# Kernel optimization log

Hardware: AMD Instinct MI355X
Metric: run time of the kernel (lower is better)

The kernel has to match this reference:

```python
import jax, jax.numpy as jnp
import numpy as np
import math

H, E, HD = 12, 768, 64   # heads, embed_dim, per-head hidden
B, S, L = 8, 512, 512    # batch, dec len, enc len
EPS = 1e-12


def layer_norm(x, w, b):
    u = jnp.mean(x, axis=-1, keepdims=True)
    s = jnp.mean((x - u) ** 2, axis=-1, keepdims=True)
    return w * (x - u) / jnp.sqrt(s + EPS) + b


def gelu(x):
    return x * 0.5 * (1.0 + jax.lax.erf(x / math.sqrt(2.0)))


def attention(k, q, w_k, w_q, pw, pb, mask):
    # k:[b,kl,E] q:[b,ql,E] w_k/w_q:[H,E,HD] mask broadcastable to [b,H,ql,kl]
    kx = jnp.einsum('ble,hed->bhld', k, w_k)
    qx = jnp.einsum('bqe,hed->bhqd', q, w_q)
    score = jnp.einsum('bhqd,bhkd->bhqk', qx, kx) / math.sqrt(HD)
    score = jnp.where(mask, score, jnp.asarray(-1e4, score.dtype))
    attn = jax.nn.softmax(score, axis=-1)
    out = jnp.einsum('bhqk,bhkd->bhqd', attn, kx)  # values are kx (as in source)
    b_, h, ql, d = out.shape
    out = out.transpose(0, 2, 1, 3).reshape(b_, ql, h * d)
    return out @ pw + pb


def setup_inputs() -> dict:
    key = jax.random.key(0)
    ks = jax.random.split(key, 16)
    xav = lambda k, shp, fan: jax.random.normal(k, shp, jnp.float32) * math.sqrt(2.0 / fan)
    inp = {
        'X': jax.random.normal(ks[0], (B, S, E), jnp.float32),
        'enc_outputs': jax.random.normal(ks[1], (B, L, E), jnp.float32),
        'enc_valid_lens': jax.random.randint(ks[2], (B,), 1, L + 1, jnp.int32),
        'w_kx1': xav(ks[3], (H, E, HD), E + HD),
        'w_qx1': xav(ks[4], (H, E, HD), E + HD),
        'proj1_w': xav(ks[5], (H * HD, E), 2 * E),
        'proj1_b': jnp.zeros((E,), jnp.float32),
        'ln1_w': jnp.ones((E,), jnp.float32),
        'ln1_b': jnp.zeros((E,), jnp.float32),
        'w_kx2': xav(ks[6], (H, E, HD), E + HD),
        'w_qx2': xav(ks[7], (H, E, HD), E + HD),
        'proj2_w': xav(ks[8], (H * HD, E), 2 * E),
        'proj2_b': jnp.zeros((E,), jnp.float32),
        'ln2_w': jnp.ones((E,), jnp.float32),
        'ln2_b': jnp.zeros((E,), jnp.float32),
        'ffn_w1': xav(ks[9], (E, E), 2 * E),
        'ffn_b1': jnp.zeros((E,), jnp.float32),
        'ffn_w2': xav(ks[10], (E, E), 2 * E),
        'ffn_b2': jnp.zeros((E,), jnp.float32),
        'ln3_w': jnp.ones((E,), jnp.float32),
        'ln3_b': jnp.zeros((E,), jnp.float32),
    }
    return inp


def reference(X, enc_outputs, enc_valid_lens,
              w_kx1, w_qx1, proj1_w, proj1_b, ln1_w, ln1_b,
              w_kx2, w_qx2, proj2_w, proj2_b, ln2_w, ln2_b,
              ffn_w1, ffn_b1, ffn_w2, ffn_b2, ln3_w, ln3_b):
    s = X.shape[1]
    # training path: dec_valid_lens is 2D -> causal mask in Attention
    causal = jnp.tril(jnp.ones((s, s), dtype=bool))[None, None]          # [1,1,s,s]
    X2 = attention(X, X, w_kx1, w_qx1, proj1_w, proj1_b, causal)
    Y = layer_norm(X2 + X, ln1_w, ln1_b)
    # cross mask: key padding from enc_valid_lens (1D branch)
    kl = enc_outputs.shape[1]
    pad = (jnp.arange(kl)[None] < enc_valid_lens[:, None])[:, None, None]  # [b,1,1,kl]
    Y2 = attention(enc_outputs, Y, w_kx2, w_qx2, proj2_w, proj2_b, pad)
    Z = layer_norm(Y2 + Y, ln2_w, ln2_b)
    F = gelu(Z @ ffn_w1 + ffn_b1) @ ffn_w2 + ffn_b2
    return layer_norm(F + Z, ln3_w, ln3_b)
```

## Files before the change

### kernel.cpp

```cpp
#include <hip/hip_runtime.h>
#include <hip/hip_bf16.h>

typedef __hip_bfloat16 bf16;
typedef __attribute__((ext_vector_type(8))) short s8v;
typedef __attribute__((ext_vector_type(4))) short s4v;
typedef __attribute__((ext_vector_type(4))) float f4v;

#define H_ 12
#define E_ 768
#define HD_ 64
#define B_ 8
#define S_ 512
#define M_ 4096

struct P9 { const void* s[8]; bf16* d[8]; const void* vs[10]; bf16* vd[10]; };

typedef __attribute__((address_space(3))) void lds_void;
typedef const __attribute__((address_space(1))) void g_void;

__device__ __forceinline__ void async_copy16(const bf16* g, short* l) {
    __builtin_amdgcn_global_load_lds((g_void*)g, (lds_void*)l, 16, 0, 0);
}

__device__ __forceinline__ float sh2f(short v) {
    unsigned int u = ((unsigned int)(unsigned short)v) << 16;
    return __uint_as_float(u);
}

__device__ __forceinline__ short f2sh(float v) {
    bf16 b = __float2bfloat16(v);
    return *(short*)&b;
}

__global__ void detect_kernel(const unsigned int* __restrict__ X, int* flag) {
    __shared__ int cnt;
    if (threadIdx.x == 0) cnt = 0;
    __syncthreads();
    int good = 0;
    for (int i = threadIdx.x; i < 16384; i += 256) {
        unsigned e = (X[i] >> 7) & 0xFFu;
        good += (e >= 100u && e <= 141u) ? 1 : 0;
    }
    atomicAdd(&cnt, good);
    __syncthreads();
    if (threadIdx.x == 0) *flag = (cnt > 9830) ? 0 : 1;
}

__global__ void conv2_kernel(const void* s0, const void* s1, bf16* d0, bf16* d1,
                             const int* __restrict__ flag) {
    const int fp32 = *flag;
    const void* s = blockIdx.y ? s1 : s0;
    bf16* d = blockIdx.y ? d1 : d0;
    int i = (blockIdx.x * 256 + threadIdx.x) * 4;
    if (fp32) {
        float4 v = *(const float4*)((const float*)s + i);
        bf16 a = __float2bfloat16(v.x), b = __float2bfloat16(v.y),
             c = __float2bfloat16(v.z), e = __float2bfloat16(v.w);
        s4v o = { *(short*)&a, *(short*)&b, *(short*)&c, *(short*)&e };
        *(s4v*)(d + i) = o;
    } else {
        *(s4v*)(d + i) = *(const s4v*)((const bf16*)s + i);
    }
}

__device__ __forceinline__ bf16 ldcvt(const void* s, int i, int fp32) {
    return fp32 ? __float2bfloat16(((const float*)s)[i]) : ((const bf16*)s)[i];
}

__global__ void repack_kernel(P9 p, const int* __restrict__ flag) {
    const int fp32 = *flag;
    const int z = blockIdx.z;
    if (z == 8) {
        int id = blockIdx.y * 12 + blockIdx.x;
        if (id < 10) {
            const void* s = p.vs[id];
            bf16* d = p.vd[id];
            for (int i = threadIdx.x; i < E_; i += 256) d[i] = ldcvt(s, i, fp32);
        }
        return;
    }
    __shared__ float t[64][65];
    const int c = threadIdx.x & 63, r0 = threadIdx.x >> 6;
    if (z < 4) {
        const void* s = p.s[z];
        bf16* d = p.d[z];
        const int e0 = blockIdx.x * 64, h = blockIdx.y;
        #pragma unroll
        for (int j = 0; j < 16; ++j) {
            int r = r0 * 16 + j;
            int idx = (h * E_ + e0 + r) * HD_ + c;
            t[r][c] = fp32 ? ((const float*)s)[idx] : __bfloat162float(((const bf16*)s)[idx]);
        }
        __syncthreads();
        #pragma unroll
        for (int j = 0; j < 16; ++j) {
            int r = r0 * 16 + j;
            d[(size_t)(h * 64 + r) * E_ + e0 + c] = __float2bfloat16(t[c][r]);
        }
    } else {
        const void* s = p.s[z];
        bf16* d = p.d[z];
        const int k0 = blockIdx.x * 64, n0 = blockIdx.y * 64;
        #pragma unroll
        for (int j = 0; j < 16; ++j) {
            int r = r0 * 16 + j;
            int idx = (k0 + r) * E_ + n0 + c;
            t[r][c] = fp32 ? ((const float*)s)[idx] : __bfloat162float(((const bf16*)s)[idx]);
        }
        __syncthreads();
        #pragma unroll
        for (int j = 0; j < 16; ++j) {
            int r = r0 * 16 + j;
            d[(size_t)(n0 + r) * E_ + k0 + c] = __float2bfloat16(t[c][r]);
        }
    }
}

template <int EPI>
__global__ __launch_bounds__(256, 4) void gemm3(const bf16* __restrict__ A,
                                                const bf16* __restrict__ Bt,
                                                bf16* __restrict__ C,
                                                const bf16* __restrict__ bias,
                                                const bf16* __restrict__ res) {
    __shared__ short As[64 * 64];
    __shared__ short Bs[64 * 64];
    const int bm = blockIdx.x, bn = blockIdx.y;
    const int tid = threadIdx.x;
    const int w = tid >> 6, l = tid & 63;
    const int wr = (w >> 1) * 32, wc = (w & 1) * 32;
    const int lc = l & 15, quad = l >> 4;
    const int srA = l >> 3, slot = l & 7;
    const int kc = (slot ^ srA) * 8;

    f4v acc[2][2] = {};

    for (int k0 = 0; k0 < E_; k0 += 64) {
        #pragma unroll
        for (int c = 0; c < 2; ++c) {
            int seg = w * 2 + c;
            int row = seg * 8 + srA;
            async_copy16(A + (size_t)(bm * 64 + row) * E_ + k0 + kc, &As[seg * 512]);
            async_copy16(Bt + (size_t)(bn * 64 + row) * E_ + k0 + kc, &Bs[seg * 512]);
        }
        __syncthreads();

        #pragma unroll
        for (int kk = 0; kk < 2; ++kk) {
            s8v a[2], b[2];
            #pragma unroll
            for (int t = 0; t < 2; ++t) {
                int ar = wr + t * 16 + lc;
                a[t] = *(const s8v*)&As[ar * 64 + (((kk * 4 + quad) ^ (ar & 7)) * 8)];
                int bc = wc + t * 16 + lc;
                b[t] = *(const s8v*)&Bs[bc * 64 + (((kk * 4 + quad) ^ (bc & 7)) * 8)];
            }
            acc[0][0] = __builtin_amdgcn_mfma_f32_16x16x32_bf16(a[0], b[0], acc[0][0], 0, 0, 0);
            acc[0][1] = __builtin_amdgcn_mfma_f32_16x16x32_bf16(a[0], b[1], acc[0][1], 0, 0, 0);
            acc[1][0] = __builtin_amdgcn_mfma_f32_16x16x32_bf16(a[1], b[0], acc[1][0], 0, 0, 0);
            acc[1][1] = __builtin_amdgcn_mfma_f32_16x16x32_bf16(a[1], b[1], acc[1][1], 0, 0, 0);
        }
        __syncthreads();
    }

    #pragma unroll
    for (int mt = 0; mt < 2; ++mt)
        #pragma unroll
        for (int nt = 0; nt < 2; ++nt)
            #pragma unroll
            for (int i = 0; i < 4; ++i) {
                int row = bm * 64 + wr + mt * 16 + quad * 4 + i;
                int col = bn * 64 + wc + nt * 16 + lc;
                float v = acc[mt][nt][i];
                if (EPI == 1)
                    v += __bfloat162float(bias[col]) + __bfloat162float(res[(size_t)row * E_ + col]);
                if (EPI == 2) {
                    v += __bfloat162float(bias[col]);
                    v = 0.5f * v * (1.0f + erff(v * 0.70710678118654752f));
                }
                C[(size_t)row * E_ + col] = __float2bfloat16(v);
            }
}

__global__ __launch_bounds__(256, 4) void gemm3q(const bf16* __restrict__ Xc,
                                                 const bf16* __restrict__ ENCc,
                                                 const bf16* __restrict__ Bt,
                                                 bf16* __restrict__ K1,
                                                 bf16* __restrict__ Q1,
                                                 bf16* __restrict__ K2,
                                                 bf16* __restrict__ KT1,
                                                 bf16* __restrict__ KT2) {
    __shared__ short sm[8192];
    short* As = sm;
    short* Bs = sm + 4096;
    const int bm = blockIdx.x, bn = blockIdx.y;
    const int tid = threadIdx.x;
    const int w = tid >> 6, l = tid & 63;
    const int wr = (w >> 1) * 32, wc = (w & 1) * 32;
    const int lc = l & 15, quad = l >> 4;
    const int srA = l >> 3, slot = l & 7;
    const int kc = (slot ^ srA) * 8;

    const bf16* A = (bn >= 24) ? ENCc : Xc;

    f4v acc[2][2] = {};

    for (int k0 = 0; k0 < E_; k0 += 64) {
        #pragma unroll
        for (int c = 0; c < 2; ++c) {
            int seg = w * 2 + c;
            int row = seg * 8 + srA;
            async_copy16(A + (size_t)(bm * 64 + row) * E_ + k0 + kc, &As[seg * 512]);
            async_copy16(Bt + (size_t)(bn * 64 + row) * E_ + k0 + kc, &Bs[seg * 512]);
        }
        __syncthreads();

        #pragma unroll
        for (int kk = 0; kk < 2; ++kk) {
            s8v a[2], b[2];
            #pragma unroll
            for (int t = 0; t < 2; ++t) {
                int ar = wr + t * 16 + lc;
                a[t] = *(const s8v*)&As[ar * 64 + (((kk * 4 + quad) ^ (ar & 7)) * 8)];
                int bc = wc + t * 16 + lc;
                b[t] = *(const s8v*)&Bs[bc * 64 + (((kk * 4 + quad) ^ (bc & 7)) * 8)];
            }
            acc[0][0] = __builtin_amdgcn_mfma_f32_16x16x32_bf16(a[0], b[0], acc[0][0], 0, 0, 0);
            acc[0][1] = __builtin_amdgcn_mfma_f32_16x16x32_bf16(a[0], b[1], acc[0][1], 0, 0, 0);
            acc[1][0] = __builtin_amdgcn_mfma_f32_16x16x32_bf16(a[1], b[0], acc[1][0], 0, 0, 0);
            acc[1][1] = __builtin_amdgcn_mfma_f32_16x16x32_bf16(a[1], b[1], acc[1][1], 0, 0, 0);
        }
        __syncthreads();
    }

    const int band = (bn < 12) ? 0 : (bn < 24) ? 1 : 2;
    const int nb = bn - band * 12;
    bf16* C = (band == 0) ? K1 : (band == 1) ? Q1 : K2;

    #pragma unroll
    for (int mt = 0; mt < 2; ++mt)
        #pragma unroll
        for (int nt = 0; nt < 2; ++nt)
            #pragma unroll
            for (int i = 0; i < 4; ++i) {
                int row = bm * 64 + wr + mt * 16 + quad * 4 + i;
                int col = nb * 64 + wc + nt * 16 + lc;
                C[(size_t)row * E_ + col] = __float2bfloat16(acc[mt][nt][i]);
            }

    if (band != 1) {
        bf16* KT = (band == 0) ? KT1 : KT2;
        #pragma unroll
        for (int mt = 0; mt < 2; ++mt)
            #pragma unroll
            for (int nt = 0; nt < 2; ++nt)
                #pragma unroll
                for (int i = 0; i < 4; ++i) {
                    int srow = wr + mt * 16 + quad * 4 + i;
                    int d = wc + nt * 16 + lc;
                    sm[d * 72 + srow] = f2sh(acc[mt][nt][i]);
                }
        __syncthreads();
        const int drow = tid >> 2, c0 = (tid & 3) * 16;
        s8v o0 = *(const s8v*)&sm[drow * 72 + c0];
        s8v o1 = *(const s8v*)&sm[drow * 72 + c0 + 8];
        const int b = bm >> 3, s0 = (bm & 7) * 64;
        bf16* dp = KT + ((size_t)((b * H_ + nb) * 64 + drow) * S_) + s0 + c0;
        *(s8v*)dp = o0;
        *(s8v*)(dp + 8) = o1;
    }
}

template <bool CAUSAL>
__global__ __launch_bounds__(256) void attn_kernel(const bf16* __restrict__ Q,
                                                   const bf16* __restrict__ Kx,
                                                   const bf16* __restrict__ KT,
                                                   bf16* __restrict__ O,
                                                   const int* __restrict__ vlen) {
    __shared__ short qs[64 * 64];
    __shared__ short ks[64 * 64];
    __shared__ short kts[64 * 64];
    __shared__ short ps[64 * 72];

    const int bh = blockIdx.x, qt = blockIdx.y;
    const int h = bh % H_, b = bh / H_;
    const int tid = threadIdx.x, w = tid >> 6, l = tid & 63;
    const int lr = (l >> 4) * 4, lc = l & 15, quad = l >> 4;
    const int srA = l >> 3, slot = l & 7;
    const int kc = (slot ^ srA) * 8;
    const int rq = w * 16 + lc;

    #pragma unroll
    for (int c = 0; c < 2; ++c) {
        int seg = w * 2 + c;
        int row = seg * 8 + srA;
        async_copy16(Q + ((size_t)(b * S_ + qt * 64 + row) * H_ + h) * HD_ + kc, &qs[seg * 512]);
    }

    const int valid = CAUSAL ? S_ : vlen[b];
    const int kmax = CAUSAL ? (qt + 1) : ((valid + 63) >> 6);

    float m_i[4], l_i[4];
    for (int i = 0; i < 4; i++) { m_i[i] = -3.0e38f; l_i[i] = 0.0f; }
    f4v o_acc[4] = {};
    s8v aq0, aq1;

    for (int kt = 0; kt < kmax; ++kt) {
        #pragma unroll
        for (int c = 0; c < 2; ++c) {
            int seg = w * 2 + c;
            int row = seg * 8 + srA;
            async_copy16(Kx + ((size_t)(b * S_ + kt * 64 + row) * H_ + h) * HD_ + kc, &ks[seg * 512]);
            async_copy16(KT + (size_t)(bh * 64 + row) * S_ + kt * 64 + kc, &kts[seg * 512]);
        }
        __syncthreads();

        if (kt == 0) {
            aq0 = *(const s8v*)&qs[rq * 64 + ((quad ^ (rq & 7)) * 8)];
            aq1 = *(const s8v*)&qs[rq * 64 + (((4 + quad) ^ (rq & 7)) * 8)];
        }

        f4v sacc[4] = {};
        #pragma unroll
        for (int nt = 0; nt < 4; nt++) {
            int rk = nt * 16 + lc;
            s8v bk0 = *(const s8v*)&ks[rk * 64 + ((quad ^ (rk & 7)) * 8)];
            s8v bk1 = *(const s8v*)&ks[rk * 64 + (((4 + quad) ^ (rk & 7)) * 8)];
            sacc[nt] = __builtin_amdgcn_mfma_f32_16x16x32_bf16(aq0, bk0, sacc[nt], 0, 0, 0);
            sacc[nt] = __builtin_amdgcn_mfma_f32_16x16x32_bf16(aq1, bk1, sacc[nt], 0, 0, 0);
        }

        #pragma unroll
        for (int i = 0; i < 4; i++) {
            int qabs = qt * 64 + w * 16 + lr + i;
            float sv[4];
            float mx = -3.0e38f;
            #pragma unroll
            for (int nt = 0; nt < 4; nt++) {
                int kabs = kt * 64 + nt * 16 + lc;
                float s = sacc[nt][i] * 0.125f;
                bool ok = CAUSAL ? (kabs <= qabs) : (kabs < valid);
                sv[nt] = ok ? s : -1.0e4f;
                mx = fmaxf(mx, sv[nt]);
            }
            #pragma unroll
            for (int off = 1; off < 16; off <<= 1) mx = fmaxf(mx, __shfl_xor(mx, off));
            float mnew = fmaxf(m_i[i], mx);
            float alpha = __expf(m_i[i] - mnew);
            float psum = 0.0f;
            #pragma unroll
            for (int nt = 0; nt < 4; nt++) {
                float p = __expf(sv[nt] - mnew);
                psum += p;
                ps[(w * 16 + lr + i) * 72 + nt * 16 + lc] = f2sh(p);
            }
            #pragma unroll
            for (int off = 1; off < 16; off <<= 1) psum += __shfl_xor(psum, off);
            l_i[i] = l_i[i] * alpha + psum;
            m_i[i] = mnew;
            #pragma unroll
            for (int dt = 0; dt < 4; dt++) o_acc[dt][i] *= alpha;
        }

        s8v ap0 = *(const s8v*)&ps[rq * 72 + quad * 8];
        s8v ap1 = *(const s8v*)&ps[rq * 72 + 32 + quad * 8];
        #pragma unroll
        for (int dt = 0; dt < 4; dt++) {
            int rd = dt * 16 + lc;
            s8v bv0 = *(const s8v*)&kts[rd * 64 + ((quad ^ (rd & 7)) * 8)];
            s8v bv1 = *(const s8v*)&kts[rd * 64 + (((4 + quad) ^ (rd & 7)) * 8)];
            o_acc[dt] = __builtin_amdgcn_mfma_f32_16x16x32_bf16(ap0, bv0, o_acc[dt], 0, 0, 0);
            o_acc[dt] = __builtin_amdgcn_mfma_f32_16x16x32_bf16(ap1, bv1, o_acc[dt], 0, 0, 0);
        }
        __syncthreads();
    }

    #pragma unroll
    for (int dt = 0; dt < 4; dt++)
        #pragma unroll
        for (int i = 0; i < 4; i++) {
            int q = qt * 64 + w * 16 + lr + i;
            int d = dt * 16 + lc;
            float v = o_acc[dt][i] / l_i[i];
            O[((size_t)(b * S_ + q) * H_ + h) * HD_ + d] = __float2bfloat16(v);
        }
}

__global__ __launch_bounds__(256) void ln2_kernel(const bf16* __restrict__ X,
                                                  const bf16* __restrict__ wv,
                                                  const bf16* __restrict__ bv,
                                                  bf16* __restrict__ outb,
                                                  float* __restrict__ outf,
                                                  const int* __restrict__ flag) {
    const int row = blockIdx.x * 4 + (threadIdx.x >> 6);
    const int l = threadIdx.x & 63;
    const bf16* xr = X + (size_t)row * E_;
    s8v v8 = *(const s8v*)(xr + l * 8);
    s4v v4 = *(const s4v*)(xr + 512 + l * 4);
    float x[12];
    #pragma unroll
    for (int j = 0; j < 8; ++j) x[j] = sh2f(v8[j]);
    #pragma unroll
    for (int j = 0; j < 4; ++j) x[8 + j] = sh2f(v4[j]);
    float s = 0.f, ss = 0.f;
    #pragma unroll
    for (int j = 0; j < 12; ++j) { s += x[j]; ss += x[j] * x[j]; }
    #pragma unroll
    for (int off = 1; off < 64; off <<= 1) {
        s += __shfl_xor(s, off);
        ss += __shfl_xor(ss, off);
    }
    float mu = s * (1.0f / E_);
    float var = ss * (1.0f / E_) - mu * mu;
    float rstd = rsqrtf(fmaxf(var, 0.0f) + 1e-12f);
    const bool f32out = (outf != nullptr) && (*flag != 0);
    #pragma unroll
    for (int j = 0; j < 12; ++j) {
        int c = (j < 8) ? (l * 8 + j) : (512 + l * 4 + (j - 8));
        float v = (x[j] - mu) * rstd * __bfloat162float(wv[c]) + __bfloat162float(bv[c]);
        if (f32out) outf[(size_t)row * E_ + c] = v;
        else        outb[(size_t)row * E_ + c] = __float2bfloat16(v);
    }
}

extern "C" void kernel_launch(void* const* d_in, const int* in_sizes, int n_in,
                              void* d_out, int out_size, void* d_ws, size_t ws_size,
                              hipStream_t stream) {
    const void* X = d_in[0];
    const void* enc = d_in[1];
    const int* vlen = (const int*)d_in[2];

    char* ws = (char*)d_ws;
    int* flag = (int*)ws;
    bf16* vecs = (bf16*)(ws + 256);
    char* wbase = ws + 16384;
    const size_t WSZ = (size_t)E_ * E_ * sizeof(bf16);
    bf16* wk1 = (bf16*)(wbase + 0 * WSZ);
    bf16* wq1 = (bf16*)(wbase + 1 * WSZ);
    bf16* wk2 = (bf16*)(wbase + 2 * WSZ);
    bf16* wq2 = (bf16*)(wbase + 3 * WSZ);
    bf16* p1t = (bf16*)(wbase + 4 * WSZ);
    bf16* p2t = (bf16*)(wbase + 5 * WSZ);
    bf16* f1t = (bf16*)(wbase + 6 * WSZ);
    bf16* f2t = (bf16*)(wbase + 7 * WSZ);
    const size_t ASZ = (size_t)M_ * E_ * sizeof(bf16);
    char* abase = wbase + 8 * WSZ;
    bf16* Xc   = (bf16*)(abase + 0 * ASZ);
    bf16* ENCc = (bf16*)(abase + 1 * ASZ);
    bf16* A0  = (bf16*)(abase + 2 * ASZ);
    bf16* A1  = (bf16*)(abase + 3 * ASZ);
    bf16* A2  = (bf16*)(abase + 4 * ASZ);
    bf16* A3  = (bf16*)(abase + 5 * ASZ);
    bf16* A4  = (bf16*)(abase + 6 * ASZ);
    bf16* A5  = (bf16*)(abase + 7 * ASZ);
    bf16* KT1 = (bf16*)(abase + 8 * ASZ);
    bf16* KT2 = (bf16*)(abase + 9 * ASZ);

    bf16* bias1 = vecs + 0 * E_;
    bf16* lw1   = vecs + 1 * E_;
    bf16* lb1   = vecs + 2 * E_;
    bf16* bias2 = vecs + 3 * E_;
    bf16* lw2   = vecs + 4 * E_;
    bf16* lb2   = vecs + 5 * E_;
    bf16* fb1   = vecs + 6 * E_;
    bf16* fb2   = vecs + 7 * E_;
    bf16* lw3   = vecs + 8 * E_;
    bf16* lb3   = vecs + 9 * E_;

    detect_kernel<<<1, 256, 0, stream>>>((const unsigned int*)X, flag);
    conv2_kernel<<<dim3(M_ * E_ / 1024, 2), 256, 0, stream>>>(X, enc, Xc, ENCc, flag);

    P9 rp;
    rp.s[0] = d_in[3];  rp.d[0] = wk1;
    rp.s[1] = d_in[4];  rp.d[1] = wq1;
    rp.s[2] = d_in[9];  rp.d[2] = wk2;
    rp.s[3] = d_in[10]; rp.d[3] = wq2;
    rp.s[4] = d_in[5];  rp.d[4] = p1t;
    rp.s[5] = d_in[11]; rp.d[5] = p2t;
    rp.s[6] = d_in[15]; rp.d[6] = f1t;
    rp.s[7] = d_in[17]; rp.d[7] = f2t;
    rp.vs[0] = d_in[6];  rp.vd[0] = bias1;
    rp.vs[1] = d_in[7];  rp.vd[1] = lw1;
    rp.vs[2] = d_in[8];  rp.vd[2] = lb1;
    rp.vs[3] = d_in[12]; rp.vd[3] = bias2;
    rp.vs[4] = d_in[13]; rp.vd[4] = lw2;
    rp.vs[5] = d_in[14]; rp.vd[5] = lb2;
    rp.vs[6] = d_in[16]; rp.vd[6] = fb1;
    rp.vs[7] = d_in[18]; rp.vd[7] = fb2;
    rp.vs[8] = d_in[19]; rp.vd[8] = lw3;
    rp.vs[9] = d_in[20]; rp.vd[9] = lb3;
    repack_kernel<<<dim3(12, 12, 9), 256, 0, stream>>>(rp, flag);

    gemm3q<<<dim3(64, 36), 256, 0, stream>>>(Xc, ENCc, wk1, A0, A1, A4, KT1, KT2);

    attn_kernel<true><<<dim3(96, 8), 256, 0, stream>>>(A1, A0, KT1, A2, nullptr);
    gemm3<1><<<dim3(64, 12), 256, 0, stream>>>(A2, p1t, A3, bias1, Xc);
    ln2_kernel<<<M_ / 4, 256, 0, stream>>>(A3, lw1, lb1, A5, nullptr, flag);

    gemm3<0><<<dim3(64, 12), 256, 0, stream>>>(A5, wq2, A1, nullptr, nullptr);
    attn_kernel<false><<<dim3(96, 8), 256, 0, stream>>>(A1, A4, KT2, A2, vlen);
    gemm3<1><<<dim3(64, 12), 256, 0, stream>>>(A2, p2t, A3, bias2, A5);
    ln2_kernel<<<M_ / 4, 256, 0, stream>>>(A3, lw2, lb2, A0, nullptr, flag);

    gemm3<2><<<dim3(64, 12), 256, 0, stream>>>(A0, f1t, A1, fb1, nullptr);
    gemm3<1><<<dim3(64, 12), 256, 0, stream>>>(A1, f2t, A2, fb2, A0);
    ln2_kernel<<<M_ / 4, 256, 0, stream>>>(A2, lw3, lb3, (bf16*)d_out, (float*)d_out, flag);
}
```

Before: 294.1 us.

## Fuse prep kernels and inline cross-attention Q projection into attention kernel

Merges dtype detection, input conversion and weight repacking into one prep kernel. Each block now recomputes the fp32 detection from a reduced 256-word sample instead of reading a flag written by a separate kernel. The cross-attention Q projection GEMM is folded into the attention kernel, which computes its 64x64 Q tile from the LayerNorm output and Wq via MFMA before the KV loop. This removes several launches and one activation round trip through global memory. In exchange, the smaller detection sample changes the heuristic, and each attention block repeats the 768-deep projection without sharing it.

```diff
diff --git a/kernel.cpp b/kernel.cpp
--- a/kernel.cpp
+++ b/kernel.cpp
@@ -32,59 +32,67 @@
     return *(short*)&b;
 }
 
-__global__ void detect_kernel(const unsigned int* __restrict__ X, int* flag) {
-    __shared__ int cnt;
-    if (threadIdx.x == 0) cnt = 0;
+__device__ __forceinline__ int detect_fp32(const unsigned int* __restrict__ Xh,
+                                           int tid, int* scratch) {
+    unsigned e = (Xh[tid] >> 7) & 0xFFu;
+    int good = (e >= 100u && e <= 141u) ? 1 : 0;
+    #pragma unroll
+    for (int off = 1; off < 64; off <<= 1) good += __shfl_xor(good, off);
+    if ((tid & 63) == 0) scratch[tid >> 6] = good;
     __syncthreads();
-    int good = 0;
-    for (int i = threadIdx.x; i < 16384; i += 256) {
-        unsigned e = (X[i] >> 7) & 0xFFu;
-        good += (e >= 100u && e <= 141u) ? 1 : 0;
-    }
-    atomicAdd(&cnt, good);
-    __syncthreads();
-    if (threadIdx.x == 0) *flag = (cnt > 9830) ? 0 : 1;
-}
-
-__global__ void conv2_kernel(const void* s0, const void* s1, bf16* d0, bf16* d1,
-                             const int* __restrict__ flag) {
-    const int fp32 = *flag;
-    const void* s = blockIdx.y ? s1 : s0;
-    bf16* d = blockIdx.y ? d1 : d0;
-    int i = (blockIdx.x * 256 + threadIdx.x) * 4;
-    if (fp32) {
-        float4 v = *(const float4*)((const float*)s + i);
-        bf16 a = __float2bfloat16(v.x), b = __float2bfloat16(v.y),
-             c = __float2bfloat16(v.z), e = __float2bfloat16(v.w);
-        s4v o = { *(short*)&a, *(short*)&b, *(short*)&c, *(short*)&e };
-        *(s4v*)(d + i) = o;
-    } else {
-        *(s4v*)(d + i) = *(const s4v*)((const bf16*)s + i);
-    }
+    int total = scratch[0] + scratch[1] + scratch[2] + scratch[3];
+    return (total <= 154) ? 1 : 0;
 }
 
 __device__ __forceinline__ bf16 ldcvt(const void* s, int i, int fp32) {
     return fp32 ? __float2bfloat16(((const float*)s)[i]) : ((const bf16*)s)[i];
 }
 
-__global__ void repack_kernel(P9 p, const int* __restrict__ flag) {
-    const int fp32 = *flag;
-    const int z = blockIdx.z;
+__global__ __launch_bounds__(256) void prep_kernel(const void* X, const void* enc,
+                                                   bf16* Xc, bf16* ENCc,
+                                                   P9 p) {
+    __shared__ int dsc[4];
+    __shared__ float t[64][65];
+    const int tid = threadIdx.x;
+    const int fp32 = detect_fp32((const unsigned int*)X, tid, dsc);
+    const int id = blockIdx.x;
+
+    if (id < 6144) {
+        const void* s = (id < 3072) ? X : enc;
+        bf16* d = (id < 3072) ? Xc : ENCc;
+        int cid = (id < 3072) ? id : id - 3072;
+        int i = (cid * 256 + tid) * 4;
+        if (fp32) {
+            float4 v = *(const float4*)((const float*)s + i);
+            bf16 a = __float2bfloat16(v.x), b = __float2bfloat16(v.y),
+                 c = __float2bfloat16(v.z), e = __float2bfloat16(v.w);
+            s4v o = { *(short*)&a, *(short*)&b, *(short*)&c, *(short*)&e };
+            *(s4v*)(d + i) = o;
+        } else {
+            *(s4v*)(d + i) = *(const s4v*)((const bf16*)s + i);
+        }
+        return;
+    }
+
+    int id2 = id - 6144;
+    const int z = id2 / 144;
+    const int rem = id2 % 144;
+    const int bx = rem % 12, by = rem / 12;
+
     if (z == 8) {
-        int id = blockIdx.y * 12 + blockIdx.x;
-        if (id < 10) {
-            const void* s = p.vs[id];
-            bf16* d = p.vd[id];
-            for (int i = threadIdx.x; i < E_; i += 256) d[i] = ldcvt(s, i, fp32);
+        int vid = by * 12 + bx;
+        if (vid < 10) {
+            const void* s = p.vs[vid];
+            bf16* d = p.vd[vid];
+            for (int i = tid; i < E_; i += 256) d[i] = ldcvt(s, i, fp32);
         }
         return;
     }
-    __shared__ float t[64][65];
-    const int c = threadIdx.x & 63, r0 = threadIdx.x >> 6;
+    const int c = tid & 63, r0 = tid >> 6;
     if (z < 4) {
         const void* s = p.s[z];
         bf16* d = p.d[z];
-        const int e0 = blockIdx.x * 64, h = blockIdx.y;
+        const int e0 = bx * 64, h = by;
         #pragma unroll
         for (int j = 0; j < 16; ++j) {
             int r = r0 * 16 + j;
@@ -100,7 +108,7 @@
     } else {
         const void* s = p.s[z];
         bf16* d = p.d[z];
-        const int k0 = blockIdx.x * 64, n0 = blockIdx.y * 64;
+        const int k0 = bx * 64, n0 = by * 64;
         #pragma unroll
         for (int j = 0; j < 16; ++j) {
             int r = r0 * 16 + j;
@@ -270,8 +278,9 @@
     }
 }
 
-template <bool CAUSAL>
+template <bool CAUSAL, bool INLQ>
 __global__ __launch_bounds__(256) void attn_kernel(const bf16* __restrict__ Q,
+                                                   const bf16* __restrict__ Wq,
                                                    const bf16* __restrict__ Kx,
                                                    const bf16* __restrict__ KT,
                                                    bf16* __restrict__ O,
@@ -289,11 +298,55 @@
     const int kc = (slot ^ srA) * 8;
     const int rq = w * 16 + lc;
 
-    #pragma unroll
-    for (int c = 0; c < 2; ++c) {
-        int seg = w * 2 + c;
-        int row = seg * 8 + srA;
-        async_copy16(Q + ((size_t)(b * S_ + qt * 64 + row) * H_ + h) * HD_ + kc, &qs[seg * 512]);
+    if (INLQ) {
+        const int wr = (w >> 1) * 32, wc = (w & 1) * 32;
+        const bf16* Arow = Q + (size_t)(b * S_ + qt * 64) * E_;
+        const bf16* Brow = Wq + (size_t)(h * 64) * E_;
+        f4v qacc[2][2] = {};
+        for (int k0 = 0; k0 < E_; k0 += 64) {
+            #pragma unroll
+            for (int c = 0; c < 2; ++c) {
+                int seg = w * 2 + c;
+                int row = seg * 8 + srA;
+                async_copy16(Arow + (size_t)row * E_ + k0 + kc, &ks[seg * 512]);
+                async_copy16(Brow + (size_t)row * E_ + k0 + kc, &kts[seg * 512]);
+            }
+            __syncthreads();
+            #pragma unroll
+            for (int kk = 0; kk < 2; ++kk) {
+                s8v a[2], bb[2];
+                #pragma unroll
+                for (int t = 0; t < 2; ++t) {
+                    int ar = wr + t * 16 + lc;
+                    a[t] = *(const s8v*)&ks[ar * 64 + (((kk * 4 + quad) ^ (ar & 7)) * 8)];
+                    int bc = wc + t * 16 + lc;
+                    bb[t] = *(const s8v*)&kts[bc * 64 + (((kk * 4 + quad) ^ (bc & 7)) * 8)];
+                }
+                qacc[0][0] = __builtin_amdgcn_mfma_f32_16x16x32_bf16(a[0], bb[0], qacc[0][0], 0, 0, 0);
+                qacc[0][1] = __builtin_amdgcn_mfma_f32_16x16x32_bf16(a[0], bb[1], qacc[0][1], 0, 0, 0);
+                qacc[1][0] = __builtin_amdgcn_mfma_f32_16x16x32_bf16(a[1], bb[0], qacc[1][0], 0, 0, 0);
+                qacc[1][1] = __builtin_amdgcn_mfma_f32_16x16x32_bf16(a[1], bb[1], qacc[1][1], 0, 0, 0);
+            }
+            __syncthreads();
+        }
+        #pragma unroll
+        for (int mt = 0; mt < 2; ++mt)
+            #pragma unroll
+            for (int nt = 0; nt < 2; ++nt)
+                #pragma unroll
+                for (int i = 0; i < 4; ++i) {
+                    int row = wr + mt * 16 + quad * 4 + i;
+                    int d = wc + nt * 16 + lc;
+                    qs[row * 64 + (((d >> 3) ^ (row & 7)) * 8) + (d & 7)] = f2sh(qacc[mt][nt][i]);
+                }
+        __syncthreads();
+    } else {
+        #pragma unroll
+        for (int c = 0; c < 2; ++c) {
+            int seg = w * 2 + c;
+            int row = seg * 8 + srA;
+            async_copy16(Q + ((size_t)(b * S_ + qt * 64 + row) * H_ + h) * HD_ + kc, &qs[seg * 512]);
+        }
     }
 
     const int valid = CAUSAL ? S_ : vlen[b];
@@ -390,7 +443,11 @@
                                                   const bf16* __restrict__ bv,
                                                   bf16* __restrict__ outb,
                                                   float* __restrict__ outf,
-                                                  const int* __restrict__ flag) {
+                                                  const unsigned int* __restrict__ Xhead) {
+    __shared__ int dsc[4];
+    int f32out = 0;
+    if (outf != nullptr)
+        f32out = detect_fp32(Xhead, threadIdx.x, dsc);
     const int row = blockIdx.x * 4 + (threadIdx.x >> 6);
     const int l = threadIdx.x & 63;
     const bf16* xr = X + (size_t)row * E_;
@@ -412,7 +469,6 @@
     float mu = s * (1.0f / E_);
     float var = ss * (1.0f / E_) - mu * mu;
     float rstd = rsqrtf(fmaxf(var, 0.0f) + 1e-12f);
-    const bool f32out = (outf != nullptr) && (*flag != 0);
     #pragma unroll
     for (int j = 0; j < 12; ++j) {
         int c = (j < 8) ? (l * 8 + j) : (512 + l * 4 + (j - 8));
@@ -430,7 +486,6 @@
     const int* vlen = (const int*)d_in[2];
 
     char* ws = (char*)d_ws;
-    int* flag = (int*)ws;
     bf16* vecs = (bf16*)(ws + 256);
     char* wbase = ws + 16384;
     const size_t WSZ = (size_t)E_ * E_ * sizeof(bf16);
@@ -466,9 +521,6 @@
     bf16* lw3   = vecs + 8 * E_;
     bf16* lb3   = vecs + 9 * E_;
 
-    detect_kernel<<<1, 256, 0, stream>>>((const unsigned int*)X, flag);
-    conv2_kernel<<<dim3(M_ * E_ / 1024, 2), 256, 0, stream>>>(X, enc, Xc, ENCc, flag);
-
     P9 rp;
     rp.s[0] = d_in[3];  rp.d[0] = wk1;
     rp.s[1] = d_in[4];  rp.d[1] = wq1;
@@ -488,20 +540,21 @@
     rp.vs[7] = d_in[18]; rp.vd[7] = fb2;
     rp.vs[8] = d_in[19]; rp.vd[8] = lw3;
     rp.vs[9] = d_in[20]; rp.vd[9] = lb3;
-    repack_kernel<<<dim3(12, 12, 9), 256, 0, stream>>>(rp, flag);
+
+    prep_kernel<<<7440, 256, 0, stream>>>(X, enc, Xc, ENCc, rp);
 
     gemm3q<<<dim3(64, 36), 256, 0, stream>>>(Xc, ENCc, wk1, A0, A1, A4, KT1, KT2);
 
-    attn_kernel<true><<<dim3(96, 8), 256, 0, stream>>>(A1, A0, KT1, A2, nullptr);
+    attn_kernel<true, false><<<dim3(96, 8), 256, 0, stream>>>(A1, nullptr, A0, KT1, A2, nullptr);
     gemm3<1><<<dim3(64, 12), 256, 0, stream>>>(A2, p1t, A3, bias1, Xc);
-    ln2_kernel<<<M_ / 4, 256, 0, stream>>>(A3, lw1, lb1, A5, nullptr, flag);
-
-    gemm3<0><<<dim3(64, 12), 256, 0, stream>>>(A5, wq2, A1, nullptr, nullptr);
-    attn_kernel<false><<<dim3(96, 8), 256, 0, stream>>>(A1, A4, KT2, A2, vlen);
+    ln2_kernel<<<M_ / 4, 256, 0, stream>>>(A3, lw1, lb1, A5, nullptr, nullptr);
+
+    attn_kernel<false, true><<<dim3(96, 8), 256, 0, stream>>>(A5, wq2, A4, KT2, A2, vlen);
     gemm3<1><<<dim3(64, 12), 256, 0, stream>>>(A2, p2t, A3, bias2, A5);
-    ln2_kernel<<<M_ / 4, 256, 0, stream>>>(A3, lw2, lb2, A0, nullptr, flag);
+    ln2_kernel<<<M_ / 4, 256, 0, stream>>>(A3, lw2, lb2, A0, nullptr, nullptr);
 
     gemm3<2><<<dim3(64, 12), 256, 0, stream>>>(A0, f1t, A1, fb1, nullptr);
     gemm3<1><<<dim3(64, 12), 256, 0, stream>>>(A1, f2t, A2, fb2, A0);
-    ln2_kernel<<<M_ / 4, 256, 0, stream>>>(A2, lw3, lb3, (bf16*)d_out, (float*)d_out, flag);
-}
+    ln2_kernel<<<M_ / 4, 256, 0, stream>>>(A2, lw3, lb3, (bf16*)d_out, (float*)d_out,
+                                           (const unsigned int*)X);
+}
```

Result: faster. 280.1 us (-4.7%).
